# Performance work log

Measured on AMD Instinct MI355X. Metric: run time of the kernel, lower is better.

## Reference

```python
import jax, jax.numpy as jnp
import numpy as np

N = 10000        # nodes
E = 320000       # edges (before self-loops)
F_IN = 128       # num_feature
H1, C1 = 16, 16  # GAT1: heads=16, out=16 -> concat 256
D = 256          # GAT2: heads=1, out=256
G = 64           # graphs in batch
L = 10           # num_label
NEG_SLOPE = 0.2


def setup_inputs() -> dict:
    key = jax.random.key(0)
    ks = jax.random.split(key, 13)
    sc = lambda f: 1.0 / np.sqrt(f)
    inp = {
        "x": jax.random.normal(ks[0], (N, F_IN), jnp.float32),
        "edge_index": jax.random.randint(ks[1], (2, E), 0, N, dtype=jnp.int32),
        "batch": jnp.sort(jax.random.randint(ks[2], (N,), 0, G, dtype=jnp.int32)),
        "W1": jax.random.normal(ks[3], (F_IN, H1 * C1), jnp.float32) * sc(F_IN),
        "a_src1": jax.random.normal(ks[4], (H1, C1), jnp.float32) * sc(C1),
        "a_dst1": jax.random.normal(ks[5], (H1, C1), jnp.float32) * sc(C1),
        "b1": jnp.zeros((H1 * C1,), jnp.float32),
        "W2": jax.random.normal(ks[6], (H1 * C1, D), jnp.float32) * sc(H1 * C1),
        "a_src2": jax.random.normal(ks[7], (1, D), jnp.float32) * sc(D),
        "a_dst2": jax.random.normal(ks[8], (1, D), jnp.float32) * sc(D),
        "b2": jnp.zeros((D,), jnp.float32),
        "lin_w": jax.random.normal(ks[9], (D, L), jnp.float32) * sc(D),
        "lin_b": jnp.zeros((L,), jnp.float32),
    }
    return inp


def _leaky(v):
    return jnp.where(v >= 0, v, NEG_SLOPE * v)


def gat_conv(x, src, dst, W, a_src, a_dst, bias, heads, ch):
    """PyG GATConv (eval mode): gather, leaky-relu logits, segment softmax over dst, scatter-add."""
    n = x.shape[0]
    h = (x @ W).reshape(n, heads, ch)                       # [N,H,C]
    al_s = jnp.sum(h * a_src, axis=-1)                      # [N,H]
    al_d = jnp.sum(h * a_dst, axis=-1)                      # [N,H]
    e = _leaky(al_s[src] + al_d[dst])                       # [Etot,H]
    m = jax.ops.segment_max(e, dst, num_segments=n)         # [N,H]
    m = jnp.where(jnp.isfinite(m), m, 0.0)
    ex = jnp.exp(e - m[dst])
    s = jax.ops.segment_sum(ex, dst, num_segments=n)        # [N,H] (>0: self-loops)
    alpha = ex / s[dst]                                     # [Etot,H]
    out = jax.ops.segment_sum(alpha[:, :, None] * h[src], dst, num_segments=n)
    return out.reshape(n, heads * ch) + bias


def reference(x, edge_index, batch, W1, a_src1, a_dst1, b1, W2, a_src2, a_dst2, b2, lin_w, lin_b):
    n = x.shape[0]
    loops = jnp.arange(n, dtype=edge_index.dtype)
    src = jnp.concatenate([edge_index[0], loops])           # add_self_loops=True (PyG default)
    dst = jnp.concatenate([edge_index[1], loops])

    h = gat_conv(x, src, dst, W1, a_src1, a_dst1, b1, H1, C1)
    h = jax.nn.relu(h)
    h = gat_conv(h, src, dst, W2, a_src2, a_dst2, b2, 1, D)

    # global_mean_pool over graph ids
    sums = jax.ops.segment_sum(h, batch, num_segments=G)    # [G,D]
    cnts = jax.ops.segment_sum(jnp.ones((n,), h.dtype), batch, num_segments=G)
    pooled = sums / jnp.maximum(cnts, 1.0)[:, None]

    # dropout is identity in eval mode
    return pooled @ lin_w + lin_b                           # [G,L]
```

## Files before the change

### kernel.cpp

```cpp
#include <hip/hip_runtime.h>
#include <hip/hip_bf16.h>
#include <math.h>

#define NEG_SLOPE 0.2f
#define LDS_FENCE() asm volatile("s_waitcnt lgkmcnt(0)" ::: "memory")

#define CSR_NB 128
#define CSR_CAP 2048
#define WT_NB 64

__device__ __forceinline__ ushort f2bf(float f) {
    uint x = __float_as_uint(f);
    x += 0x7fffu + ((x >> 16) & 1u);
    return (ushort)(x >> 16);
}
__device__ __forceinline__ float bf2f(ushort u) {
    return __uint_as_float((uint)u << 16);
}

typedef __attribute__((ext_vector_type(8))) short bf16x8v;
typedef __attribute__((ext_vector_type(4))) float f32x4;

__device__ __forceinline__ void gemm1_body(float* __restrict__ ws, int bx,
    const float* __restrict__ X, const float* __restrict__ W,
    ushort* __restrict__ Cb, const float* __restrict__ a_src,
    const float* __restrict__ a_dst, float* __restrict__ als,
    float* __restrict__ ald, int N) {
    const int K = 128;
    int t = threadIdx.x;
    int lane = t & 63, wave = t >> 6;
    int n0 = bx * 16 + wave * 4;
    const float* Xr[4];
#pragma unroll
    for (int rr = 0; rr < 4; ++rr) {
        int r = min(n0 + rr, N - 1);
        Xr[rr] = X + (size_t)__builtin_amdgcn_readfirstlane(r) * K;
    }
    float4 acc[4] = {};
    for (int kt = 0; kt < K; kt += 32) {
        const float4* Wg = (const float4*)(W + (size_t)kt * 256);
        float4* wsv = (float4*)ws;
#pragma unroll
        for (int i = 0; i < 8; ++i) wsv[t + i * 256] = Wg[t + i * 256];
        __syncthreads();
#pragma unroll 4
        for (int kk = 0; kk < 32; kk += 4) {
            int k = kt + kk;
            float4 w0 = *(const float4*)&ws[(size_t)(kk + 0) * 256 + lane * 4];
            float4 w1 = *(const float4*)&ws[(size_t)(kk + 1) * 256 + lane * 4];
            float4 w2 = *(const float4*)&ws[(size_t)(kk + 2) * 256 + lane * 4];
            float4 w3 = *(const float4*)&ws[(size_t)(kk + 3) * 256 + lane * 4];
#pragma unroll
            for (int rr = 0; rr < 4; ++rr) {
                float4 xv = *(const float4*)(Xr[rr] + k);
                acc[rr].x = fmaf(xv.x, w0.x, acc[rr].x);
                acc[rr].y = fmaf(xv.x, w0.y, acc[rr].y);
                acc[rr].z = fmaf(xv.x, w0.z, acc[rr].z);
                acc[rr].w = fmaf(xv.x, w0.w, acc[rr].w);
                acc[rr].x = fmaf(xv.y, w1.x, acc[rr].x);
                acc[rr].y = fmaf(xv.y, w1.y, acc[rr].y);
                acc[rr].z = fmaf(xv.y, w1.z, acc[rr].z);
                acc[rr].w = fmaf(xv.y, w1.w, acc[rr].w);
                acc[rr].x = fmaf(xv.z, w2.x, acc[rr].x);
                acc[rr].y = fmaf(xv.z, w2.y, acc[rr].y);
                acc[rr].z = fmaf(xv.z, w2.z, acc[rr].z);
                acc[rr].w = fmaf(xv.z, w2.w, acc[rr].w);
                acc[rr].x = fmaf(xv.w, w3.x, acc[rr].x);
                acc[rr].y = fmaf(xv.w, w3.y, acc[rr].y);
                acc[rr].z = fmaf(xv.w, w3.z, acc[rr].z);
                acc[rr].w = fmaf(xv.w, w3.w, acc[rr].w);
            }
        }
        __syncthreads();
    }
    if (n0 >= N) return;
    float4 asv = *(const float4*)(a_src + lane * 4);
    float4 adv = *(const float4*)(a_dst + lane * 4);
#pragma unroll
    for (int rr = 0; rr < 4; ++rr) {
        int n = n0 + rr;
        if (n >= N) break;
        ushort4 u;
        u.x = f2bf(acc[rr].x); u.y = f2bf(acc[rr].y);
        u.z = f2bf(acc[rr].z); u.w = f2bf(acc[rr].w);
        *(ushort4*)(Cb + (size_t)n * 256 + lane * 4) = u;
        float s = acc[rr].x * asv.x + acc[rr].y * asv.y + acc[rr].z * asv.z + acc[rr].w * asv.w;
        float d = acc[rr].x * adv.x + acc[rr].y * adv.y + acc[rr].z * adv.z + acc[rr].w * adv.w;
        s += __shfl_xor(s, 1); s += __shfl_xor(s, 2);
        d += __shfl_xor(d, 1); d += __shfl_xor(d, 2);
        if ((lane & 3) == 0) {
            als[n * 16 + (lane >> 2)] = s;
            ald[n * 16 + (lane >> 2)] = d;
        }
    }
}

__global__ __launch_bounds__(256) void k_scatter_gemm1(
    const int* __restrict__ ei, int E, int N, int NP, int CE,
    int* __restrict__ gcount, int* __restrict__ tmp,
    const float* __restrict__ X, const float* __restrict__ W1, ushort* __restrict__ A,
    const float* __restrict__ as1, const float* __restrict__ ad1,
    float* __restrict__ als1, float* __restrict__ ald1,
    const float* __restrict__ W2, ushort* __restrict__ Wt) {
    __shared__ float smem[32 * 256];
    int t = threadIdx.x;
    if (blockIdx.x < CSR_NB) {
        int* lhist = (int*)smem;
        int b = blockIdx.x;
        for (int p = t; p < 384; p += 256) lhist[p] = 0;
        __syncthreads();
        int Etot = E + N;
        int e0 = b * CE, e1 = min(Etot, e0 + CE);
        for (int e = e0 + t; e < e1; e += 256) {
            int d = (e < E) ? ei[E + e] : (e - E);
            atomicAdd(&lhist[d >> 5], 1);
        }
        __syncthreads();
        for (int p = t; p < NP; p += 256) {
            int c = lhist[p];
            lhist[p] = c ? atomicAdd(&gcount[p], c) : 0;
        }
        __syncthreads();
        for (int e = e0 + t; e < e1; e += 256) {
            int s, d;
            if (e < E) { s = ei[e]; d = ei[E + e]; } else { s = d = e - E; }
            int p = d >> 5;
            int pos = atomicAdd(&lhist[p], 1);
            tmp[p * CSR_CAP + min(pos, CSR_CAP - 1)] = (s << 5) | (d & 31);
        }
    } else if (blockIdx.x < CSR_NB + WT_NB) {
        float (*tile)[33] = (float (*)[33])smem;
        int tb = blockIdx.x - CSR_NB;
        int k0 = (tb >> 3) * 32, j0 = (tb & 7) * 32;
        int c = t & 31, i0 = t >> 5;
#pragma unroll
        for (int p = 0; p < 4; ++p) {
            int i = i0 + p * 8;
            tile[i][c] = W2[(size_t)(k0 + i) * 256 + j0 + c];
        }
        __syncthreads();
#pragma unroll
        for (int p = 0; p < 4; ++p) {
            int i = i0 + p * 8;
            Wt[(size_t)(j0 + i) * 256 + k0 + c] = f2bf(tile[c][i]);
        }
    } else {
        gemm1_body(smem, blockIdx.x - CSR_NB - WT_NB, X, W1, A, as1, ad1, als1, ald1, N);
    }
}

__global__ __launch_bounds__(256) void k_gemm2_mfma(
    const ushort* __restrict__ Xb, const ushort* __restrict__ Wt,
    ushort* __restrict__ Cb, const float* __restrict__ as2,
    const float* __restrict__ ad2, float* __restrict__ als,
    float* __restrict__ ald, int N) {
    __shared__ float red[4][16][2];
    int t = threadIdx.x, lane = t & 63, w = t >> 6;
    int n0 = blockIdx.x * 16;
    int l15 = lane & 15, kb = lane >> 4;
    int col0 = w * 64;
    int arow = min(n0 + l15, N - 1);
    const ushort* Xp = Xb + (size_t)arow * 256 + kb * 8;
    f32x4 acc[4] = {f32x4{0,0,0,0}, f32x4{0,0,0,0}, f32x4{0,0,0,0}, f32x4{0,0,0,0}};
#pragma unroll
    for (int ks = 0; ks < 8; ++ks) {
        bf16x8v a = *(const bf16x8v*)(Xp + ks * 32);
#pragma unroll
        for (int tt = 0; tt < 4; ++tt) {
            const ushort* Bp = Wt + (size_t)(col0 + tt * 16 + l15) * 256 + ks * 32 + kb * 8;
            bf16x8v b = *(const bf16x8v*)Bp;
            acc[tt] = __builtin_amdgcn_mfma_f32_16x16x32_bf16(a, b, acc[tt], 0, 0, 0);
        }
    }
#pragma unroll
    for (int r = 0; r < 4; ++r) {
        int n = n0 + kb * 4 + r;
        float s = 0.f, d = 0.f;
#pragma unroll
        for (int tt = 0; tt < 4; ++tt) {
            int col = col0 + tt * 16 + l15;
            float v = acc[tt][r];
            if (n < N) Cb[(size_t)n * 256 + col] = f2bf(v);
            s += v * as2[col];
            d += v * ad2[col];
        }
        s += __shfl_xor(s, 1); s += __shfl_xor(s, 2);
        s += __shfl_xor(s, 4); s += __shfl_xor(s, 8);
        d += __shfl_xor(d, 1); d += __shfl_xor(d, 2);
        d += __shfl_xor(d, 4); d += __shfl_xor(d, 8);
        if (l15 == 0) { red[w][kb * 4 + r][0] = s; red[w][kb * 4 + r][1] = d; }
    }
    __syncthreads();
    if (t < 16) {
        int n = n0 + t;
        if (n < N) {
            als[n] = red[0][t][0] + red[1][t][0] + red[2][t][0] + red[3][t][0];
            ald[n] = red[0][t][1] + red[1][t][1] + red[2][t][1] + red[3][t][1];
        }
    }
}

__global__ __launch_bounds__(256) void k_csr_final(const int* __restrict__ tmp,
                                                   const int* __restrict__ gcount,
                                                   int2* __restrict__ rowse,
                                                   int* __restrict__ col, int N) {
    __shared__ int dcnt[32], dcur[32];
    int t = threadIdx.x, p = blockIdx.x;
    int base = p * CSR_CAP;
    int cnt = min(gcount[p], CSR_CAP);
    if (t < 32) dcnt[t] = 0;
    __syncthreads();
    for (int i = t; i < cnt; i += 256) atomicAdd(&dcnt[tmp[base + i] & 31], 1);
    __syncthreads();
    if (t < 32) {
        int v = dcnt[t];
        int x = v;
#pragma unroll
        for (int off = 1; off < 32; off <<= 1) {
            int u = __shfl_up(x, off);
            if (t >= off) x += u;
        }
        int excl = x - v;
        dcur[t] = excl;
        int dst = (p << 5) + t;
        if (dst < N) rowse[dst] = make_int2(base + excl, base + excl + v);
    }
    __syncthreads();
    for (int i = t; i < cnt; i += 256) {
        int v = tmp[base + i];
        int pos = atomicAdd(&dcur[v & 31], 1);
        col[base + pos] = v >> 5;
    }
}

__global__ __launch_bounds__(256) void k_gather_h1(
    const int2* __restrict__ rowse, const int* __restrict__ col,
    const ushort* __restrict__ Hb, const float* __restrict__ als,
    const float* __restrict__ ald, const float* __restrict__ bias,
    ushort* __restrict__ outb, int N) {
    int wave = threadIdx.x >> 6, lane = threadIdx.x & 63;
    int n = blockIdx.x * 4 + wave;
    if (n >= N) return;
    int2 se2 = rowse[n];
    int start = se2.x, end = se2.y;
    float aldv = ald[n];
    float4 acc = {0.f, 0.f, 0.f, 0.f};
    float swsum = 0.f;
    const ushort* Hl = Hb + lane * 4;
    for (int base = start; base < end; base += 64) {
        int len = min(64, end - base);
        int s_r = 0;
        float w_r = 0.f;
        if (lane < len) {
            s_r = col[base + lane];
            float v = als[s_r] + aldv;
            v = v >= 0.f ? v : NEG_SLOPE * v;
            w_r = __expf(v);
        }
        swsum += w_r;
        int len8 = (len + 7) & ~7;
        for (int e = 0; e < len8; e += 8) {
            const ushort* hp[8];
            float we[8];
#pragma unroll
            for (int j = 0; j < 8; ++j) {
                hp[j] = Hl + (size_t)__shfl(s_r, e + j) * 256;
                we[j] = __shfl(w_r, e + j);
            }
            ushort4 uv[8];
#pragma unroll
            for (int j = 0; j < 8; ++j) uv[j] = *(const ushort4*)hp[j];
#pragma unroll
            for (int j = 0; j < 8; ++j) {
                acc.x = fmaf(we[j], bf2f(uv[j].x), acc.x);
                acc.y = fmaf(we[j], bf2f(uv[j].y), acc.y);
                acc.z = fmaf(we[j], bf2f(uv[j].z), acc.z);
                acc.w = fmaf(we[j], bf2f(uv[j].w), acc.w);
            }
        }
    }
#pragma unroll
    for (int off = 32; off >= 1; off >>= 1) swsum += __shfl_xor(swsum, off);
    float inv = 1.0f / swsum;
    float4 bv = *(const float4*)(bias + lane * 4);
    ushort4 o;
    o.x = f2bf(fmaf(acc.x, inv, bv.x));
    o.y = f2bf(fmaf(acc.y, inv, bv.y));
    o.z = f2bf(fmaf(acc.z, inv, bv.z));
    o.w = f2bf(fmaf(acc.w, inv, bv.w));
    *(ushort4*)(outb + (size_t)n * 256 + lane * 4) = o;
}

__global__ __launch_bounds__(256) void k_gather_h16(
    const int2* __restrict__ rowse, const int* __restrict__ col,
    const ushort* __restrict__ Hb, const float* __restrict__ als,
    const float* __restrict__ ald, const float* __restrict__ bias,
    ushort* __restrict__ outb, int N) {
    __shared__ float w_lds[4][64 * 16];
    int wave = threadIdx.x >> 6, lane = threadIdx.x & 63;
    int n = blockIdx.x * 4 + wave;
    if (n >= N) return;
    int2 se2 = rowse[n];
    int start = se2.x, end = se2.y;
    int hq = lane & 15;
    int eq = lane >> 4;
    float aldW = ald[n * 16 + hq];
    float4 acc = {0.f, 0.f, 0.f, 0.f};
    float swp = 0.f;
    const ushort* Hl = Hb + lane * 4;
    for (int base = start; base < end; base += 64) {
        int len = min(64, end - base);
        int s_r = (lane < len) ? col[base + lane] : 0;
#pragma unroll
        for (int k = 0; k < 16; ++k) {
            int esub = (k << 2) + eq;
            int s = __shfl(s_r, esub);
            float w = 0.f;
            if (esub < len) {
                float v = als[s * 16 + hq] + aldW;
                v = v >= 0.f ? v : NEG_SLOPE * v;
                w = __expf(v);
            }
            w_lds[wave][(esub << 4) + hq] = w;
            swp += w;
        }
        LDS_FENCE();
        int len8 = (len + 7) & ~7;
        for (int e = 0; e < len8; e += 8) {
            const ushort* hp[8];
            float we[8];
#pragma unroll
            for (int j = 0; j < 8; ++j) {
                hp[j] = Hl + (size_t)__shfl(s_r, e + j) * 256;
                we[j] = w_lds[wave][((e + j) << 4) + (lane >> 2)];
            }
            ushort4 uv[8];
#pragma unroll
            for (int j = 0; j < 8; ++j) uv[j] = *(const ushort4*)hp[j];
#pragma unroll
            for (int j = 0; j < 8; ++j) {
                acc.x = fmaf(we[j], bf2f(uv[j].x), acc.x);
                acc.y = fmaf(we[j], bf2f(uv[j].y), acc.y);
                acc.z = fmaf(we[j], bf2f(uv[j].z), acc.z);
                acc.w = fmaf(we[j], bf2f(uv[j].w), acc.w);
            }
        }
        LDS_FENCE();
    }
    swp += __shfl_xor(swp, 16);
    swp += __shfl_xor(swp, 32);
    float inv = 1.0f / __shfl(swp, lane >> 2);
    float4 bv = *(const float4*)(bias + lane * 4);
    ushort4 o;
    o.x = f2bf(fmaxf(fmaf(acc.x, inv, bv.x), 0.f));
    o.y = f2bf(fmaxf(fmaf(acc.y, inv, bv.y), 0.f));
    o.z = f2bf(fmaxf(fmaf(acc.z, inv, bv.z), 0.f));
    o.w = f2bf(fmaxf(fmaf(acc.w, inv, bv.w), 0.f));
    *(ushort4*)(outb + (size_t)n * 256 + lane * 4) = o;
}

__device__ __forceinline__ int lower_bound_i(const int* __restrict__ a, int n, int v) {
    int lo = 0, hi = n;
    while (lo < hi) {
        int mid = (lo + hi) >> 1;
        if (a[mid] < v) lo = mid + 1; else hi = mid;
    }
    return lo;
}

__global__ __launch_bounds__(1024) void k_pool_final(const ushort* __restrict__ Bb,
                                                     const int* __restrict__ batch,
                                                     const float* __restrict__ lw,
                                                     const float* __restrict__ lb,
                                                     float* __restrict__ out,
                                                     int N, int L) {
    __shared__ float psum[4][256];
    __shared__ float csum[256];
    int t = threadIdx.x;
    int c = t & 255, q = t >> 8;
    int g = blockIdx.x;
    int lo = lower_bound_i(batch, N, g);
    int hi = lower_bound_i(batch, N, g + 1);
    int len = hi - lo;
    int per = (len + 3) >> 2;
    int s0 = lo + q * per, s1 = min(hi, s0 + per);
    float acc = 0.f;
    for (int r = s0; r < s1; ++r) acc += bf2f(Bb[(size_t)r * 256 + c]);
    psum[q][c] = acc;
    __syncthreads();
    if (t < 256) csum[t] = psum[0][t] + psum[1][t] + psum[2][t] + psum[3][t];
    __syncthreads();
    int wave = t >> 6, lane = t & 63;
    if (wave < L) {
        int l = wave;
        float a = csum[lane] * lw[lane * L + l] +
                  csum[lane + 64] * lw[(lane + 64) * L + l] +
                  csum[lane + 128] * lw[(lane + 128) * L + l] +
                  csum[lane + 192] * lw[(lane + 192) * L + l];
#pragma unroll
        for (int off = 32; off >= 1; off >>= 1) a += __shfl_xor(a, off);
        if (lane == 0) out[g * L + l] = a / fmaxf((float)len, 1.0f) + lb[l];
    }
}

extern "C" void kernel_launch(void* const* d_in, const int* in_sizes, int n_in,
                              void* d_out, int out_size, void* d_ws, size_t ws_size,
                              hipStream_t stream) {
    const float* x   = (const float*)d_in[0];
    const int*   ei  = (const int*)d_in[1];
    const int*   bat = (const int*)d_in[2];
    const float* W1  = (const float*)d_in[3];
    const float* as1 = (const float*)d_in[4];
    const float* ad1 = (const float*)d_in[5];
    const float* b1  = (const float*)d_in[6];
    const float* W2  = (const float*)d_in[7];
    const float* as2 = (const float*)d_in[8];
    const float* ad2 = (const float*)d_in[9];
    const float* b2  = (const float*)d_in[10];
    const float* lw  = (const float*)d_in[11];
    const float* lb  = (const float*)d_in[12];
    float* out = (float*)d_out;

    const int N = in_sizes[2];
    const int E = in_sizes[1] / 2;
    const int G = 64, L = 10;
    const int Etot = E + N;
    const int NP = (N + 31) >> 5;
    const int CE = (Etot + CSR_NB - 1) / CSR_NB;

    float* A    = (float*)d_ws;
    float* B    = A + (size_t)N * 256;
    float* als1 = B + (size_t)N * 256;
    float* ald1 = als1 + (size_t)N * 16;
    float* als2 = ald1 + (size_t)N * 16;
    float* ald2 = als2 + N;
    int2* rowse = (int2*)(ald2 + N);
    int* col    = (int*)(rowse + N);
    int* tmp    = col + (size_t)NP * CSR_CAP;
    int* gcount = tmp + (size_t)NP * CSR_CAP;
    ushort* Wt  = (ushort*)(gcount + NP);
    ushort* Abf = (ushort*)A;
    ushort* Bbf = (ushort*)B;

    const int BS = 256;
    auto nb = [](int n, int b) { return (n + b - 1) / b; };
    int nodes4 = nb(N, 4);
    int rows16 = nb(N, 16);

    hipMemsetAsync(gcount, 0, NP * sizeof(int), stream);
    k_scatter_gemm1<<<CSR_NB + WT_NB + rows16, BS, 0, stream>>>(
        ei, E, N, NP, CE, gcount, tmp, x, W1, Abf, as1, ad1, als1, ald1, W2, Wt);
    k_csr_final<<<NP, BS, 0, stream>>>(tmp, gcount, rowse, col, N);

    k_gather_h16<<<nodes4, BS, 0, stream>>>(rowse, col, Abf, als1, ald1, b1, Bbf, N);

    k_gemm2_mfma<<<rows16, BS, 0, stream>>>(Bbf, Wt, Abf, as2, ad2, als2, ald2, N);
    k_gather_h1<<<nodes4, BS, 0, stream>>>(rowse, col, Abf, als2, ald2, b2, Bbf, N);

    k_pool_final<<<G, 1024, 0, stream>>>(Bbf, bat, lw, lb, out, N, L);
}
```

Before: 191.5 us.

## Move first GEMM to bf16 MFMA and fuse it with CSR finalization

Replaces the fp32 FMA-based first linear layer with a bf16 MFMA GEMM. A prep kernel now converts x to bf16 and transposes W1 to bf16 alongside the CSR bucketing, and the MFMA GEMM runs in the same launch as CSR finalization. The aim is to cut the arithmetic cost of the first GEMM while keeping the launch count unchanged. In exchange, x and W1 are rounded to bf16 (lower precision), and the attention-logit reductions now use more shuffles per output.

```diff
diff --git a/kernel.cpp b/kernel.cpp
--- a/kernel.cpp
+++ b/kernel.cpp
@@ -7,6 +7,8 @@
 
 #define CSR_NB 128
 #define CSR_CAP 2048
+#define XC_NB 128
+#define W1T_NB 32
 #define WT_NB 64
 
 __device__ __forceinline__ ushort f2bf(float f) {
@@ -21,88 +23,13 @@
 typedef __attribute__((ext_vector_type(8))) short bf16x8v;
 typedef __attribute__((ext_vector_type(4))) float f32x4;
 
-__device__ __forceinline__ void gemm1_body(float* __restrict__ ws, int bx,
-    const float* __restrict__ X, const float* __restrict__ W,
-    ushort* __restrict__ Cb, const float* __restrict__ a_src,
-    const float* __restrict__ a_dst, float* __restrict__ als,
-    float* __restrict__ ald, int N) {
-    const int K = 128;
-    int t = threadIdx.x;
-    int lane = t & 63, wave = t >> 6;
-    int n0 = bx * 16 + wave * 4;
-    const float* Xr[4];
-#pragma unroll
-    for (int rr = 0; rr < 4; ++rr) {
-        int r = min(n0 + rr, N - 1);
-        Xr[rr] = X + (size_t)__builtin_amdgcn_readfirstlane(r) * K;
-    }
-    float4 acc[4] = {};
-    for (int kt = 0; kt < K; kt += 32) {
-        const float4* Wg = (const float4*)(W + (size_t)kt * 256);
-        float4* wsv = (float4*)ws;
-#pragma unroll
-        for (int i = 0; i < 8; ++i) wsv[t + i * 256] = Wg[t + i * 256];
-        __syncthreads();
-#pragma unroll 4
-        for (int kk = 0; kk < 32; kk += 4) {
-            int k = kt + kk;
-            float4 w0 = *(const float4*)&ws[(size_t)(kk + 0) * 256 + lane * 4];
-            float4 w1 = *(const float4*)&ws[(size_t)(kk + 1) * 256 + lane * 4];
-            float4 w2 = *(const float4*)&ws[(size_t)(kk + 2) * 256 + lane * 4];
-            float4 w3 = *(const float4*)&ws[(size_t)(kk + 3) * 256 + lane * 4];
-#pragma unroll
-            for (int rr = 0; rr < 4; ++rr) {
-                float4 xv = *(const float4*)(Xr[rr] + k);
-                acc[rr].x = fmaf(xv.x, w0.x, acc[rr].x);
-                acc[rr].y = fmaf(xv.x, w0.y, acc[rr].y);
-                acc[rr].z = fmaf(xv.x, w0.z, acc[rr].z);
-                acc[rr].w = fmaf(xv.x, w0.w, acc[rr].w);
-                acc[rr].x = fmaf(xv.y, w1.x, acc[rr].x);
-                acc[rr].y = fmaf(xv.y, w1.y, acc[rr].y);
-                acc[rr].z = fmaf(xv.y, w1.z, acc[rr].z);
-                acc[rr].w = fmaf(xv.y, w1.w, acc[rr].w);
-                acc[rr].x = fmaf(xv.z, w2.x, acc[rr].x);
-                acc[rr].y = fmaf(xv.z, w2.y, acc[rr].y);
-                acc[rr].z = fmaf(xv.z, w2.z, acc[rr].z);
-                acc[rr].w = fmaf(xv.z, w2.w, acc[rr].w);
-                acc[rr].x = fmaf(xv.w, w3.x, acc[rr].x);
-                acc[rr].y = fmaf(xv.w, w3.y, acc[rr].y);
-                acc[rr].z = fmaf(xv.w, w3.z, acc[rr].z);
-                acc[rr].w = fmaf(xv.w, w3.w, acc[rr].w);
-            }
-        }
-        __syncthreads();
-    }
-    if (n0 >= N) return;
-    float4 asv = *(const float4*)(a_src + lane * 4);
-    float4 adv = *(const float4*)(a_dst + lane * 4);
-#pragma unroll
-    for (int rr = 0; rr < 4; ++rr) {
-        int n = n0 + rr;
-        if (n >= N) break;
-        ushort4 u;
-        u.x = f2bf(acc[rr].x); u.y = f2bf(acc[rr].y);
-        u.z = f2bf(acc[rr].z); u.w = f2bf(acc[rr].w);
-        *(ushort4*)(Cb + (size_t)n * 256 + lane * 4) = u;
-        float s = acc[rr].x * asv.x + acc[rr].y * asv.y + acc[rr].z * asv.z + acc[rr].w * asv.w;
-        float d = acc[rr].x * adv.x + acc[rr].y * adv.y + acc[rr].z * adv.z + acc[rr].w * adv.w;
-        s += __shfl_xor(s, 1); s += __shfl_xor(s, 2);
-        d += __shfl_xor(d, 1); d += __shfl_xor(d, 2);
-        if ((lane & 3) == 0) {
-            als[n * 16 + (lane >> 2)] = s;
-            ald[n * 16 + (lane >> 2)] = d;
-        }
-    }
-}
-
-__global__ __launch_bounds__(256) void k_scatter_gemm1(
+__global__ __launch_bounds__(256) void k_prep(
     const int* __restrict__ ei, int E, int N, int NP, int CE,
     int* __restrict__ gcount, int* __restrict__ tmp,
-    const float* __restrict__ X, const float* __restrict__ W1, ushort* __restrict__ A,
-    const float* __restrict__ as1, const float* __restrict__ ad1,
-    float* __restrict__ als1, float* __restrict__ ald1,
+    const float* __restrict__ x, ushort* __restrict__ Xb,
+    const float* __restrict__ W1, ushort* __restrict__ W1t,
     const float* __restrict__ W2, ushort* __restrict__ Wt) {
-    __shared__ float smem[32 * 256];
+    __shared__ float smem[32 * 33];
     int t = threadIdx.x;
     if (blockIdx.x < CSR_NB) {
         int* lhist = (int*)smem;
@@ -128,9 +55,35 @@
             int pos = atomicAdd(&lhist[p], 1);
             tmp[p * CSR_CAP + min(pos, CSR_CAP - 1)] = (s << 5) | (d & 31);
         }
-    } else if (blockIdx.x < CSR_NB + WT_NB) {
+    } else if (blockIdx.x < CSR_NB + XC_NB) {
+        int b = blockIdx.x - CSR_NB;
+        int nfl4 = N * 32;
+        int stride = XC_NB * 256;
+        for (int i = b * 256 + t; i < nfl4; i += stride) {
+            float4 v = ((const float4*)x)[i];
+            ushort4 u;
+            u.x = f2bf(v.x); u.y = f2bf(v.y); u.z = f2bf(v.z); u.w = f2bf(v.w);
+            ((ushort4*)Xb)[i] = u;
+        }
+    } else if (blockIdx.x < CSR_NB + XC_NB + W1T_NB) {
         float (*tile)[33] = (float (*)[33])smem;
-        int tb = blockIdx.x - CSR_NB;
+        int tb = blockIdx.x - CSR_NB - XC_NB;
+        int k0 = (tb >> 3) * 32, j0 = (tb & 7) * 32;
+        int c = t & 31, i0 = t >> 5;
+#pragma unroll
+        for (int p = 0; p < 4; ++p) {
+            int i = i0 + p * 8;
+            tile[i][c] = W1[(size_t)(k0 + i) * 256 + j0 + c];
+        }
+        __syncthreads();
+#pragma unroll
+        for (int p = 0; p < 4; ++p) {
+            int i = i0 + p * 8;
+            W1t[(size_t)(j0 + i) * 128 + k0 + c] = f2bf(tile[c][i]);
+        }
+    } else {
+        float (*tile)[33] = (float (*)[33])smem;
+        int tb = blockIdx.x - CSR_NB - XC_NB - W1T_NB;
         int k0 = (tb >> 3) * 32, j0 = (tb & 7) * 32;
         int c = t & 31, i0 = t >> 5;
 #pragma unroll
@@ -144,8 +97,92 @@
             int i = i0 + p * 8;
             Wt[(size_t)(j0 + i) * 256 + k0 + c] = f2bf(tile[c][i]);
         }
-    } else {
-        gemm1_body(smem, blockIdx.x - CSR_NB - WT_NB, X, W1, A, as1, ad1, als1, ald1, N);
+    }
+}
+
+__device__ __forceinline__ void gemm1_mfma_body(int bx,
+    const ushort* __restrict__ Xb, const ushort* __restrict__ W1t,
+    ushort* __restrict__ Cb, const float* __restrict__ as1,
+    const float* __restrict__ ad1, float* __restrict__ als,
+    float* __restrict__ ald, int N) {
+    int t = threadIdx.x, lane = t & 63, w = t >> 6;
+    int n0 = bx * 16;
+    int l15 = lane & 15, kb = lane >> 4;
+    int col0 = w * 64;
+    int arow = min(n0 + l15, N - 1);
+    const ushort* Xp = Xb + (size_t)arow * 128 + kb * 8;
+    f32x4 acc[4] = {f32x4{0,0,0,0}, f32x4{0,0,0,0}, f32x4{0,0,0,0}, f32x4{0,0,0,0}};
+#pragma unroll
+    for (int ks = 0; ks < 4; ++ks) {
+        bf16x8v a = *(const bf16x8v*)(Xp + ks * 32);
+#pragma unroll
+        for (int tt = 0; tt < 4; ++tt) {
+            const ushort* Bp = W1t + (size_t)(col0 + tt * 16 + l15) * 128 + ks * 32 + kb * 8;
+            bf16x8v b = *(const bf16x8v*)Bp;
+            acc[tt] = __builtin_amdgcn_mfma_f32_16x16x32_bf16(a, b, acc[tt], 0, 0, 0);
+        }
+    }
+#pragma unroll
+    for (int r = 0; r < 4; ++r) {
+        int n = n0 + kb * 4 + r;
+#pragma unroll
+        for (int tt = 0; tt < 4; ++tt) {
+            int col = col0 + tt * 16 + l15;
+            float v = acc[tt][r];
+            float s = v * as1[col];
+            float d = v * ad1[col];
+            s += __shfl_xor(s, 1); s += __shfl_xor(s, 2);
+            s += __shfl_xor(s, 4); s += __shfl_xor(s, 8);
+            d += __shfl_xor(d, 1); d += __shfl_xor(d, 2);
+            d += __shfl_xor(d, 4); d += __shfl_xor(d, 8);
+            if (n < N) {
+                Cb[(size_t)n * 256 + col] = f2bf(v);
+                if (l15 == 0) {
+                    als[n * 16 + (col >> 4)] = s;
+                    ald[n * 16 + (col >> 4)] = d;
+                }
+            }
+        }
+    }
+}
+
+__global__ __launch_bounds__(256) void k_g1f(
+    const int* __restrict__ tmp, const int* __restrict__ gcount,
+    int2* __restrict__ rowse, int* __restrict__ col, int NP,
+    const ushort* __restrict__ Xb, const ushort* __restrict__ W1t,
+    ushort* __restrict__ Cb, const float* __restrict__ as1,
+    const float* __restrict__ ad1, float* __restrict__ als1,
+    float* __restrict__ ald1, int N) {
+    if ((int)blockIdx.x >= NP) {
+        gemm1_mfma_body(blockIdx.x - NP, Xb, W1t, Cb, as1, ad1, als1, ald1, N);
+        return;
+    }
+    __shared__ int dcnt[32], dcur[32];
+    int t = threadIdx.x, p = blockIdx.x;
+    int base = p * CSR_CAP;
+    int cnt = min(gcount[p], CSR_CAP);
+    if (t < 32) dcnt[t] = 0;
+    __syncthreads();
+    for (int i = t; i < cnt; i += 256) atomicAdd(&dcnt[tmp[base + i] & 31], 1);
+    __syncthreads();
+    if (t < 32) {
+        int v = dcnt[t];
+        int x = v;
+#pragma unroll
+        for (int off = 1; off < 32; off <<= 1) {
+            int u = __shfl_up(x, off);
+            if (t >= off) x += u;
+        }
+        int excl = x - v;
+        dcur[t] = excl;
+        int dst = (p << 5) + t;
+        if (dst < N) rowse[dst] = make_int2(base + excl, base + excl + v);
+    }
+    __syncthreads();
+    for (int i = t; i < cnt; i += 256) {
+        int v = tmp[base + i];
+        int pos = atomicAdd(&dcur[v & 31], 1);
+        col[base + pos] = v >> 5;
     }
 }
 
@@ -197,39 +234,6 @@
             als[n] = red[0][t][0] + red[1][t][0] + red[2][t][0] + red[3][t][0];
             ald[n] = red[0][t][1] + red[1][t][1] + red[2][t][1] + red[3][t][1];
         }
-    }
-}
-
-__global__ __launch_bounds__(256) void k_csr_final(const int* __restrict__ tmp,
-                                                   const int* __restrict__ gcount,
-                                                   int2* __restrict__ rowse,
-                                                   int* __restrict__ col, int N) {
-    __shared__ int dcnt[32], dcur[32];
-    int t = threadIdx.x, p = blockIdx.x;
-    int base = p * CSR_CAP;
-    int cnt = min(gcount[p], CSR_CAP);
-    if (t < 32) dcnt[t] = 0;
-    __syncthreads();
-    for (int i = t; i < cnt; i += 256) atomicAdd(&dcnt[tmp[base + i] & 31], 1);
-    __syncthreads();
-    if (t < 32) {
-        int v = dcnt[t];
-        int x = v;
-#pragma unroll
-        for (int off = 1; off < 32; off <<= 1) {
-            int u = __shfl_up(x, off);
-            if (t >= off) x += u;
-        }
-        int excl = x - v;
-        dcur[t] = excl;
-        int dst = (p << 5) + t;
-        if (dst < N) rowse[dst] = make_int2(base + excl, base + excl + v);
-    }
-    __syncthreads();
-    for (int i = t; i < cnt; i += 256) {
-        int v = tmp[base + i];
-        int pos = atomicAdd(&dcur[v & 31], 1);
-        col[base + pos] = v >> 5;
     }
 }
 
@@ -438,7 +442,9 @@
     int* col    = (int*)(rowse + N);
     int* tmp    = col + (size_t)NP * CSR_CAP;
     int* gcount = tmp + (size_t)NP * CSR_CAP;
-    ushort* Wt  = (ushort*)(gcount + NP);
+    ushort* Wt  = (ushort*)(((uintptr_t)(gcount + NP) + 63) & ~(uintptr_t)63);
+    ushort* W1t = Wt + 256 * 256;
+    ushort* Xb  = W1t + 256 * 128;
     ushort* Abf = (ushort*)A;
     ushort* Bbf = (ushort*)B;
 
@@ -448,9 +454,11 @@
     int rows16 = nb(N, 16);
 
     hipMemsetAsync(gcount, 0, NP * sizeof(int), stream);
-    k_scatter_gemm1<<<CSR_NB + WT_NB + rows16, BS, 0, stream>>>(
-        ei, E, N, NP, CE, gcount, tmp, x, W1, Abf, as1, ad1, als1, ald1, W2, Wt);
-    k_csr_final<<<NP, BS, 0, stream>>>(tmp, gcount, rowse, col, N);
+    k_prep<<<CSR_NB + XC_NB + W1T_NB + WT_NB, BS, 0, stream>>>(
+        ei, E, N, NP, CE, gcount, tmp, x, Xb, W1, W1t, W2, Wt);
+
+    k_g1f<<<NP + rows16, BS, 0, stream>>>(tmp, gcount, rowse, col, NP,
+                                          Xb, W1t, Abf, as1, ad1, als1, ald1, N);
 
     k_gather_h16<<<nodes4, BS, 0, stream>>>(rowse, col, Abf, als1, ald1, b1, Bbf, N);
 
```

After: 195.2 us. No clear change (+1.9%).
